# Kernel tuning notes

Hardware: AMD Instinct MI355X
Metric: run time of the kernel (lower is better)

The kernel has to match this reference:

```python
import jax, jax.numpy as jnp
import numpy as np

H, W = 512, 512          # pseudo_image_dims
C = 32                   # feat_channels == MHA embed_dim
NH, HD = 2, 16           # heads, head_dim
B, NL, NR = 2, 50000, 20000
EPS = 1e-5
SCALE = np.float32(1.0 / np.sqrt(HD))

# 3x3 neighbor shifts used by shift_bev_grids (INDEX_SHIFT in source)
INDEX_SHIFT = jnp.array([[0, 0], [-1, 0], [1, 0], [0, 1], [-1, 1], [1, 1], [0, -1], [-1, -1], [1, -1]], dtype=jnp.int32)
# 5x5 shifts used by new_gen_dy_coor (gen_index_shift(2))
SHIFT25 = jnp.array([[i, j] for i in range(-2, 3) for j in range(-2, 3)], dtype=jnp.int32)


def _unique_coords(key, n):
    perm = jax.random.permutation(key, H * W)[:n]
    return jnp.stack([perm // W, perm % W], axis=1).astype(jnp.int32)


def setup_inputs():
    key = jax.random.key(0)
    ks = jax.random.split(key, 8)
    inp = {
        "li_bev_feats": jax.random.normal(ks[0], (B, NL, C), jnp.float32),
        "li_bev_coors": jnp.stack([_unique_coords(jax.random.fold_in(ks[1], b), NL) for b in range(B)]),
        "ra_bev_feats": jax.random.normal(ks[2], (B, NR, C), jnp.float32),
        "ra_bev_coors": jnp.stack([_unique_coords(jax.random.fold_in(ks[3], b), NR) for b in range(B)]),
        "radar_bev_dy": jax.random.bernoulli(ks[4], 0.3, (B, NR)),
    }
    pk = jax.random.split(ks[5], 12)
    w = lambda k, o, i: 0.05 * jax.random.normal(k, (o, i), jnp.float32)
    z = lambda n: jnp.zeros((n,), jnp.float32)
    inp.update(
        ln_li_w=jnp.ones((C,), jnp.float32), ln_li_b=z(C),
        ln_ra_w=jnp.ones((C,), jnp.float32), ln_ra_b=z(C),
        q1_w=w(pk[0], C, C), q1_b=z(C), k1_w=w(pk[1], C, C), k1_b=z(C), v1_w=w(pk[2], C, C), v1_b=z(C),
        q2_w=w(pk[3], C, C), q2_b=z(C), k2_w=w(pk[4], C, C), k2_b=z(C), v2_w=w(pk[5], C, C), v2_b=z(C),
        pos_w=w(pk[6], C, 2), pos_b=z(C),
        a1_in_w=w(pk[7], 3 * C, C), a1_in_b=z(3 * C), a1_out_w=w(pk[8], C, C), a1_out_b=z(C),
        a2_in_w=w(pk[9], 3 * C, C), a2_in_b=z(3 * C), a2_out_w=w(pk[10], C, C), a2_out_b=z(C),
    )
    return inp


def _ln(x, w, b):
    mu = jnp.mean(x, -1, keepdims=True)
    var = jnp.mean(jnp.square(x - mu), -1, keepdims=True)
    return (x - mu) / jnp.sqrt(var + EPS) * w + b


def _grid_of(coors, n):
    # dense coord -> pillar-index lookup table, -1 for empty cells
    return jnp.full((H, W), -1, jnp.int32).at[coors[:, 0], coors[:, 1]].set(jnp.arange(n, dtype=jnp.int32))


def _gather_kv(coors, grid, k_map, v_map, pe9):
    # per pillar: look up the 3x3 shifted neighbors in the OTHER modality's grid
    sh = coors[:, None, :] + INDEX_SHIFT[None]                      # [N,9,2]
    inb = (sh[..., 0] >= 0) & (sh[..., 0] < H) & (sh[..., 1] >= 0) & (sh[..., 1] < W)
    idx = grid[jnp.clip(sh[..., 0], 0, H - 1), jnp.clip(sh[..., 1], 0, W - 1)]
    valid = (inb & (idx >= 0))[..., None]                           # [N,9,1]
    safe = jnp.clip(idx, 0, None)
    k = jnp.where(valid, k_map[safe], 0.0)                          # masked_fill(~cond, 0)
    v = jnp.where(valid, v_map[safe] + pe9[None], 0.0)              # pos-enc added before masking
    return k, v


def _mha(q, k, v, Wi, bi, Wo, bo):
    # torch MultiheadAttention (batch_first, eval -> no dropout); q [N,1,C], k/v [N,9,C]
    n = q.shape[0]
    qp = (q @ Wi[:C].T + bi[:C]).reshape(n, 1, NH, HD)
    kp = (k @ Wi[C:2 * C].T + bi[C:2 * C]).reshape(n, -1, NH, HD)
    vp = (v @ Wi[2 * C:].T + bi[2 * C:]).reshape(n, -1, NH, HD)
    s = jnp.einsum("nqhd,nkhd->nhqk", qp, kp) * SCALE
    a = jax.nn.softmax(s, axis=-1)
    o = jnp.einsum("nhqk,nkhd->nqhd", a, vp).reshape(n, C)
    return o @ Wo.T + bo


def _scatter(coors, feat):
    # PointPillarsScatter: place [N,C] features at their (x,y) cells of a [C,H,W] canvas
    return jnp.zeros((H, W, C), feat.dtype).at[coors[:, 0], coors[:, 1]].set(feat).transpose(2, 0, 1)


def _forward(li_bev_feats, li_bev_coors, ra_bev_feats, ra_bev_coors, radar_bev_dy,
             ln_li_w, ln_li_b, ln_ra_w, ln_ra_b,
             q1_w, q1_b, k1_w, k1_b, v1_w, v1_b,
             q2_w, q2_b, k2_w, k2_b, v2_w, v2_b,
             pos_w, pos_b,
             a1_in_w, a1_in_b, a1_out_w, a1_out_b,
             a2_in_w, a2_in_b, a2_out_w, a2_out_b):
    pe9 = INDEX_SHIFT.astype(jnp.float32) @ pos_w.T + pos_b        # [9,C] positional codes

    def per_sample(li_f, li_c, ra_f, ra_c, ra_dy):
        li_n = _ln(li_f, ln_li_w, ln_li_b)
        ra_n = _ln(ra_f, ln_ra_w, ln_ra_b)
        li_grid = _grid_of(li_c, NL)
        ra_grid = _grid_of(ra_c, NR)
        # new_gen_dy_coor: lidar pillars within a 5x5 (mod dims+1) window of any dynamic radar pillar
        g = jnp.array([H + 1, W + 1], jnp.int32)
        sh = (ra_c[:, None, :] + SHIFT25[None]) % g                # [NR,25,2]
        inb = (sh[..., 0] < H) & (sh[..., 1] < W)
        idx = li_grid[jnp.clip(sh[..., 0], 0, H - 1), jnp.clip(sh[..., 1], 0, W - 1)]
        valid = inb & (idx >= 0) & ra_dy[:, None]
        dy_mask = jnp.zeros(NL + 1, bool).at[jnp.where(valid, idx, NL).reshape(-1)].set(True)[:NL]
        # branch 1: dynamic lidar queries cross-attend to 3x3 radar neighbors
        q1 = li_n @ q1_w.T + q1_b
        k1 = ra_n @ k1_w.T + k1_b
        v1 = ra_n @ v1_w.T + v1_b
        k, v = _gather_kv(li_c, ra_grid, k1, v1, pe9)
        out1 = _mha(q1[:, None, :], k, v, a1_in_w, a1_in_b, a1_out_w, a1_out_b)
        out1 = out1 * dy_mask[:, None].astype(out1.dtype)          # only dy pillars scattered
        img_li = _scatter(li_c, out1)
        # branch 2: radar queries cross-attend to 3x3 lidar neighbors
        q2 = ra_n @ q2_w.T + q2_b
        k2 = li_n @ k2_w.T + k2_b
        v2 = li_n @ v2_w.T + v2_b
        k, v = _gather_kv(ra_c, li_grid, k2, v2, pe9)
        out2 = _mha(q2[:, None, :], k, v, a2_in_w, a2_in_b, a2_out_w, a2_out_b)
        img_ra = _scatter(ra_c, out2)
        return img_li, img_ra

    return jax.vmap(per_sample)(li_bev_feats, li_bev_coors, ra_bev_feats, ra_bev_coors, radar_bev_dy)


def reference(li_bev_feats, li_bev_coors, ra_bev_feats, ra_bev_coors, radar_bev_dy,
              ln_li_w, ln_li_b, ln_ra_w, ln_ra_b,
              q1_w, q1_b, k1_w, k1_b, v1_w, v1_b,
              q2_w, q2_b, k2_w, k2_b, v2_w, v2_b,
              pos_w, pos_b,
              a1_in_w, a1_in_b, a1_out_w, a1_out_b,
              a2_in_w, a2_in_b, a2_out_w, a2_out_b):
    return _forward(li_bev_feats, li_bev_coors, ra_bev_feats, ra_bev_coors, radar_bev_dy,
                    ln_li_w, ln_li_b, ln_ra_w, ln_ra_b,
                    q1_w, q1_b, k1_w, k1_b, v1_w, v1_b,
                    q2_w, q2_b, k2_w, k2_b, v2_w, v2_b,
                    pos_w, pos_b,
                    a1_in_w, a1_in_b, a1_out_w, a1_out_b,
                    a2_in_w, a2_in_b, a2_out_w, a2_out_b)
```

## Files before the change

kernel.cpp:

```cpp
#include <hip/hip_runtime.h>
#include <stdint.h>

constexpr int Hh = 512, Ww = 512;
constexpr int C  = 32;
constexpr int B  = 2;
constexpr int NL = 50000;
constexpr int NR = 20000;
constexpr float EPS = 1e-5f;
constexpr float SCALE = 0.25f;

constexpr int CB_MATS = 0;
constexpr int CB_CVEC = 6144;
constexpr int CB_PE1  = 6336;
constexpr int CB_PE2  = 6624;
constexpr int CB_INV  = 6912;
constexpr int CB_TOT  = 7040;

__device__ __constant__ int DX9[9] = {0,-1,1,0,-1,1,0,-1,1};
__device__ __constant__ int DY9[9] = {0,0,0,1,1,1,-1,-1,-1};

__global__ void build_grid_k(const int* __restrict__ coors, int n, int* __restrict__ grid) {
    int b = blockIdx.y;
    int i = blockIdx.x * blockDim.x + threadIdx.x;
    if (i >= n) return;
    int x = coors[((size_t)b * n + i) * 2 + 0];
    int y = coors[((size_t)b * n + i) * 2 + 1];
    grid[(size_t)b * Hh * Ww + x * Ww + y] = i;
}

__global__ void combine_mats_k(const float* __restrict__ a1w, const float* __restrict__ a2w,
                               const float* __restrict__ q1w, const float* __restrict__ k1w,
                               const float* __restrict__ v1w, const float* __restrict__ q2w,
                               const float* __restrict__ k2w, const float* __restrict__ v2w,
                               float* __restrict__ cb) {
    int m = blockIdx.x;
    int t = threadIdx.x;
    const float* A = (m < 3 ? a1w : a2w) + (m % 3) * C * C;
    const float* Wm;
    switch (m) { case 0: Wm=q1w; break; case 1: Wm=k1w; break; case 2: Wm=v1w; break;
                 case 3: Wm=q2w; break; case 4: Wm=k2w; break; default: Wm=v2w; }
    int r = t >> 5, d = t & 31;
    float s = 0.f;
    #pragma unroll
    for (int c = 0; c < C; ++c) s += A[r * C + c] * Wm[c * C + d];
    cb[CB_MATS + m * 1024 + r * C + d] = s;
}

__global__ void combine_vecs_k(const float* __restrict__ a1w, const float* __restrict__ a1b,
                               const float* __restrict__ a2w, const float* __restrict__ a2b,
                               const float* __restrict__ q1b, const float* __restrict__ k1b,
                               const float* __restrict__ v1b, const float* __restrict__ q2b,
                               const float* __restrict__ k2b, const float* __restrict__ v2b,
                               const float* __restrict__ posw, const float* __restrict__ posb,
                               float* __restrict__ cb) {
    int t = threadIdx.x;
    if (t < 192) {
        int m = t / 32, r = t & 31;
        const float* A  = (m < 3 ? a1w : a2w) + (m % 3) * C * C;
        const float* ab = (m < 3 ? a1b : a2b) + (m % 3) * C;
        const float* bv = (m == 0 ? q1b : m == 1 ? k1b : m == 2 ? v1b
                         : m == 3 ? q2b : m == 4 ? k2b : v2b);
        float s = ab[r];
        #pragma unroll
        for (int c = 0; c < C; ++c) s += A[r * C + c] * bv[c];
        cb[CB_CVEC + m * 32 + r] = s;
    } else if (t < 480) {
        int u = t - 192; int j = u >> 5, r = u & 31;
        const float* A = a1w + 2 * C * C;
        float sx = (float)DX9[j], sy = (float)DY9[j];
        float s = 0.f;
        #pragma unroll
        for (int c = 0; c < C; ++c) {
            float pe = posw[c * 2 + 0] * sx + posw[c * 2 + 1] * sy + posb[c];
            s += A[r * C + c] * pe;
        }
        cb[CB_PE1 + j * 32 + r] = s;
    } else if (t < 768) {
        int u = t - 480; int j = u >> 5, r = u & 31;
        const float* A = a2w + 2 * C * C;
        float sx = (float)DX9[j], sy = (float)DY9[j];
        float s = 0.f;
        #pragma unroll
        for (int c = 0; c < C; ++c) {
            float pe = posw[c * 2 + 0] * sx + posw[c * 2 + 1] * sy + posb[c];
            s += A[r * C + c] * pe;
        }
        cb[CB_PE2 + j * 32 + r] = s;
    } else if (t < 896) {
        int u = t - 768; int m = u >> 5, r = u & 31;
        cb[CB_INV + u] = (m == 0 ? a1b[32 + r] : m == 1 ? a1b[64 + r]
                        : m == 2 ? a2b[32 + r] : a2b[64 + r]);
    }
}

__global__ void ln_proj_k(const float* __restrict__ feats, int n,
                          const float* __restrict__ lnw, const float* __restrict__ lnb,
                          const float* __restrict__ cb, int mq, int mk, int mv,
                          float* __restrict__ qmap, float* __restrict__ kmap,
                          float* __restrict__ vmap) {
    __shared__ float sM[3][1024];
    __shared__ float sc[3][32];
    for (int p = threadIdx.x; p < 1024; p += blockDim.x) {
        sM[0][p] = cb[CB_MATS + mq * 1024 + p];
        sM[1][p] = cb[CB_MATS + mk * 1024 + p];
        sM[2][p] = cb[CB_MATS + mv * 1024 + p];
    }
    if (threadIdx.x < 32) {
        sc[0][threadIdx.x] = cb[CB_CVEC + mq * 32 + threadIdx.x];
        sc[1][threadIdx.x] = cb[CB_CVEC + mk * 32 + threadIdx.x];
        sc[2][threadIdx.x] = cb[CB_CVEC + mv * 32 + threadIdx.x];
    }
    __syncthreads();
    int b = blockIdx.y;
    int i = blockIdx.x * blockDim.x + threadIdx.x;
    if (i >= n) return;

    float x[C];
    const float* f = feats + ((size_t)b * n + i) * C;
    float mu = 0.f;
    #pragma unroll
    for (int c = 0; c < C; ++c) { x[c] = f[c]; mu += x[c]; }
    mu *= (1.0f / C);
    float var = 0.f;
    #pragma unroll
    for (int c = 0; c < C; ++c) { float d = x[c] - mu; var += d * d; }
    var *= (1.0f / C);
    float inv = 1.0f / sqrtf(var + EPS);
    #pragma unroll
    for (int c = 0; c < C; ++c) x[c] = (x[c] - mu) * inv * lnw[c] + lnb[c];

    float* outs[3] = { qmap, kmap, vmap };
    #pragma unroll
    for (int m = 0; m < 3; ++m) {
        float* o = outs[m] + ((size_t)b * n + i) * C;
        #pragma unroll
        for (int r = 0; r < C; ++r) {
            float s = sc[m][r];
            #pragma unroll
            for (int d = 0; d < C; ++d) s += sM[m][r * C + d] * x[d];
            o[r] = s;
        }
    }
}

__global__ void dy_mask_k(const int* __restrict__ ra_coors, const int* __restrict__ ra_dy,
                          const int* __restrict__ li_grid, uint8_t* __restrict__ mask) {
    int b = blockIdx.y;
    int r = blockIdx.x * blockDim.x + threadIdx.x;
    if (r >= NR) return;
    if (ra_dy[(size_t)b * NR + r] == 0) return;
    int x = ra_coors[((size_t)b * NR + r) * 2 + 0];
    int y = ra_coors[((size_t)b * NR + r) * 2 + 1];
    #pragma unroll
    for (int dx = -2; dx <= 2; ++dx) {
        #pragma unroll
        for (int dy = -2; dy <= 2; ++dy) {
            int sx = x + dx; sx = (sx < 0) ? sx + (Hh + 1) : (sx >= Hh + 1 ? sx - (Hh + 1) : sx);
            int sy = y + dy; sy = (sy < 0) ? sy + (Ww + 1) : (sy >= Ww + 1 ? sy - (Ww + 1) : sy);
            if (sx < Hh && sy < Ww) {
                int idx = li_grid[(size_t)b * Hh * Ww + sx * Ww + sy];
                if (idx >= 0) mask[(size_t)b * NL + idx] = 1;
            }
        }
    }
}

__global__ void attn_k(const float* __restrict__ qmap, const float* __restrict__ kmap,
                       const float* __restrict__ vmap, const int* __restrict__ q_coors,
                       const int* __restrict__ kv_grid, const float* __restrict__ cb,
                       int pe_off, int kinv_off, int vinv_off,
                       const float* __restrict__ Wo, const float* __restrict__ bo,
                       const uint8_t* __restrict__ mask, float* __restrict__ canvas,
                       int nq, int nkv) {
    __shared__ float sWo[1024];
    __shared__ float sbo[32], skinv[32], svinv[32];
    __shared__ float spe[9 * 32];
    for (int p = threadIdx.x; p < 1024; p += blockDim.x) sWo[p] = Wo[p];
    if (threadIdx.x < 32) {
        sbo[threadIdx.x]   = bo[threadIdx.x];
        skinv[threadIdx.x] = cb[kinv_off + threadIdx.x];
        svinv[threadIdx.x] = cb[vinv_off + threadIdx.x];
    }
    for (int p = threadIdx.x; p < 288; p += blockDim.x) spe[p] = cb[pe_off + p];
    __syncthreads();

    int b = blockIdx.y;
    int i = blockIdx.x * blockDim.x + threadIdx.x;
    if (i >= nq) return;
    if (mask && !mask[(size_t)b * NL + i]) return;

    int x = q_coors[((size_t)b * nq + i) * 2 + 0];
    int y = q_coors[((size_t)b * nq + i) * 2 + 1];

    int nidx[9];
    #pragma unroll
    for (int j = 0; j < 9; ++j) {
        int sx = x + DX9[j], sy = y + DY9[j];
        nidx[j] = (sx >= 0 && sx < Hh && sy >= 0 && sy < Ww)
                  ? kv_grid[(size_t)b * Hh * Ww + sx * Ww + sy] : -1;
    }

    float qp[C];
    const float* qpp = qmap + ((size_t)b * nq + i) * C;
    #pragma unroll
    for (int c = 0; c < C; ++c) qp[c] = qpp[c];

    float sc0[9], sc1[9];
    #pragma unroll
    for (int j = 0; j < 9; ++j) {
        int idx = nidx[j];
        const float* kp = (idx >= 0) ? (kmap + ((size_t)b * nkv + idx) * C) : skinv;
        float s0 = 0.f, s1 = 0.f;
        #pragma unroll
        for (int d = 0; d < 16; ++d) { s0 += qp[d] * kp[d]; s1 += qp[16 + d] * kp[16 + d]; }
        sc0[j] = s0 * SCALE; sc1[j] = s1 * SCALE;
    }
    float m0 = sc0[0], m1 = sc1[0];
    #pragma unroll
    for (int j = 1; j < 9; ++j) { m0 = fmaxf(m0, sc0[j]); m1 = fmaxf(m1, sc1[j]); }
    float sum0 = 0.f, sum1 = 0.f;
    #pragma unroll
    for (int j = 0; j < 9; ++j) {
        sc0[j] = expf(sc0[j] - m0); sum0 += sc0[j];
        sc1[j] = expf(sc1[j] - m1); sum1 += sc1[j];
    }
    float r0 = 1.0f / sum0, r1 = 1.0f / sum1;

    float o[C];
    #pragma unroll
    for (int c = 0; c < C; ++c) o[c] = 0.f;
    #pragma unroll
    for (int j = 0; j < 9; ++j) {
        float a0 = sc0[j] * r0, a1 = sc1[j] * r1;
        int idx = nidx[j];
        if (idx >= 0) {
            const float* vp = vmap + ((size_t)b * nkv + idx) * C;
            #pragma unroll
            for (int d = 0; d < 16; ++d) {
                o[d]      += a0 * (vp[d]      + spe[j * 32 + d]);
                o[16 + d] += a1 * (vp[16 + d] + spe[j * 32 + 16 + d]);
            }
        } else {
            #pragma unroll
            for (int d = 0; d < 16; ++d) {
                o[d]      += a0 * svinv[d];
                o[16 + d] += a1 * svinv[16 + d];
            }
        }
    }

    size_t base = (size_t)b * C * Hh * Ww + (size_t)x * Ww + y;
    #pragma unroll
    for (int r = 0; r < C; ++r) {
        float s = sbo[r];
        #pragma unroll
        for (int c = 0; c < C; ++c) s += sWo[r * C + c] * o[c];
        canvas[base + (size_t)r * Hh * Ww] = s;
    }
}

extern "C" void kernel_launch(void* const* d_in, const int* in_sizes, int n_in,
                              void* d_out, int out_size, void* d_ws, size_t ws_size,
                              hipStream_t stream) {
    const float*   li_f  = (const float*)d_in[0];
    const int*     li_c  = (const int*)d_in[1];
    const float*   ra_f  = (const float*)d_in[2];
    const int*     ra_c  = (const int*)d_in[3];
    const int*     ra_dy = (const int*)d_in[4];
    const float* ln_li_w = (const float*)d_in[5];
    const float* ln_li_b = (const float*)d_in[6];
    const float* ln_ra_w = (const float*)d_in[7];
    const float* ln_ra_b = (const float*)d_in[8];
    const float* q1w = (const float*)d_in[9],  *q1b = (const float*)d_in[10];
    const float* k1w = (const float*)d_in[11], *k1b = (const float*)d_in[12];
    const float* v1w = (const float*)d_in[13], *v1b = (const float*)d_in[14];
    const float* q2w = (const float*)d_in[15], *q2b = (const float*)d_in[16];
    const float* k2w = (const float*)d_in[17], *k2b = (const float*)d_in[18];
    const float* v2w = (const float*)d_in[19], *v2b = (const float*)d_in[20];
    const float* posw = (const float*)d_in[21], *posb = (const float*)d_in[22];
    const float* a1iw = (const float*)d_in[23], *a1ib = (const float*)d_in[24];
    const float* a1ow = (const float*)d_in[25], *a1ob = (const float*)d_in[26];
    const float* a2iw = (const float*)d_in[27], *a2ib = (const float*)d_in[28];
    const float* a2ow = (const float*)d_in[29], *a2ob = (const float*)d_in[30];

    char* ws = (char*)d_ws;
    size_t off = 0;
    auto carve = [&](size_t bytes) { void* p = ws + off; off += (bytes + 255) & ~(size_t)255; return p; };
    int*     li_grid = (int*)carve((size_t)B * Hh * Ww * 4);
    int*     ra_grid = (int*)carve((size_t)B * Hh * Ww * 4);
    uint8_t* mask    = (uint8_t*)carve((size_t)B * NL);
    float*   cb      = (float*)carve((size_t)CB_TOT * 4);
    float*   qp1 = (float*)carve((size_t)B * NL * C * 4);
    float*   kp1 = (float*)carve((size_t)B * NR * C * 4);
    float*   vp1 = (float*)carve((size_t)B * NR * C * 4);
    float*   qp2 = (float*)carve((size_t)B * NR * C * 4);
    float*   kp2 = (float*)carve((size_t)B * NL * C * 4);
    float*   vp2 = (float*)carve((size_t)B * NL * C * 4);
    (void)ws_size; (void)n_in; (void)in_sizes;

    float* out_li = (float*)d_out;
    float* out_ra = out_li + (size_t)B * C * Hh * Ww;

    hipMemsetAsync(d_out, 0, (size_t)out_size * sizeof(float), stream);
    hipMemsetAsync(li_grid, 0xFF, (size_t)2 * B * Hh * Ww * 4, stream);
    hipMemsetAsync(mask, 0, (size_t)B * NL, stream);

    combine_mats_k<<<dim3(6), dim3(1024), 0, stream>>>(a1iw, a2iw, q1w, k1w, v1w, q2w, k2w, v2w, cb);
    combine_vecs_k<<<dim3(1), dim3(1024), 0, stream>>>(a1iw, a1ib, a2iw, a2ib,
                                                       q1b, k1b, v1b, q2b, k2b, v2b, posw, posb, cb);
    build_grid_k<<<dim3((NL + 255) / 256, B), dim3(256), 0, stream>>>(li_c, NL, li_grid);
    build_grid_k<<<dim3((NR + 255) / 256, B), dim3(256), 0, stream>>>(ra_c, NR, ra_grid);

    ln_proj_k<<<dim3((NL + 255) / 256, B), dim3(256), 0, stream>>>(li_f, NL, ln_li_w, ln_li_b,
                                                                   cb, 0, 4, 5, qp1, kp2, vp2);
    ln_proj_k<<<dim3((NR + 255) / 256, B), dim3(256), 0, stream>>>(ra_f, NR, ln_ra_w, ln_ra_b,
                                                                   cb, 3, 1, 2, qp2, kp1, vp1);
    dy_mask_k<<<dim3((NR + 255) / 256, B), dim3(256), 0, stream>>>(ra_c, ra_dy, li_grid, mask);

    attn_k<<<dim3((NL + 255) / 256, B), dim3(256), 0, stream>>>(
        qp1, kp1, vp1, li_c, ra_grid, cb, CB_PE1, CB_INV + 0, CB_INV + 32,
        a1ow, a1ob, mask, out_li, NL, NR);
    attn_k<<<dim3((NR + 255) / 256, B), dim3(256), 0, stream>>>(
        qp2, kp2, vp2, ra_c, li_grid, cb, CB_PE2, CB_INV + 64, CB_INV + 96,
        a2ow, a2ob, nullptr, out_ra, NR, NL);
}
```

Measured before the change: 384.1 us.

## Replace output memset and strided scatter with a dense gather canvas pass

Attention kernels now write compact per-pillar features, and a new canvas kernel walks every grid cell to gather features, or write zeros, into the channel-major output. This removes the full-output memset and the scattered strided canvas writes in favour of coalesced writes. It also merges the two grid-build launches and the two constant-prep launches into one each, and uses float4 loads and stores for feature rows. The cost is extra intermediate buffers plus a pass that reads both grids and the compact features.

```diff
diff --git a/kernel.cpp b/kernel.cpp
--- a/kernel.cpp
+++ b/kernel.cpp
@@ -19,51 +19,56 @@
 __device__ __constant__ int DX9[9] = {0,-1,1,0,-1,1,0,-1,1};
 __device__ __constant__ int DY9[9] = {0,0,0,1,1,1,-1,-1,-1};
 
-__global__ void build_grid_k(const int* __restrict__ coors, int n, int* __restrict__ grid) {
+__global__ void build_grids_k(const int* __restrict__ li_c, const int* __restrict__ ra_c,
+                              int* __restrict__ li_grid, int* __restrict__ ra_grid) {
     int b = blockIdx.y;
     int i = blockIdx.x * blockDim.x + threadIdx.x;
-    if (i >= n) return;
-    int x = coors[((size_t)b * n + i) * 2 + 0];
-    int y = coors[((size_t)b * n + i) * 2 + 1];
-    grid[(size_t)b * Hh * Ww + x * Ww + y] = i;
-}
-
-__global__ void combine_mats_k(const float* __restrict__ a1w, const float* __restrict__ a2w,
-                               const float* __restrict__ q1w, const float* __restrict__ k1w,
-                               const float* __restrict__ v1w, const float* __restrict__ q2w,
-                               const float* __restrict__ k2w, const float* __restrict__ v2w,
-                               float* __restrict__ cb) {
+    if (i < NL) {
+        int x = li_c[((size_t)b * NL + i) * 2 + 0];
+        int y = li_c[((size_t)b * NL + i) * 2 + 1];
+        li_grid[(size_t)b * Hh * Ww + x * Ww + y] = i;
+    } else if (i < NL + NR) {
+        int j = i - NL;
+        int x = ra_c[((size_t)b * NR + j) * 2 + 0];
+        int y = ra_c[((size_t)b * NR + j) * 2 + 1];
+        ra_grid[(size_t)b * Hh * Ww + x * Ww + y] = j;
+    }
+}
+
+__global__ void const_k(const float* __restrict__ a1w, const float* __restrict__ a1b,
+                        const float* __restrict__ a2w, const float* __restrict__ a2b,
+                        const float* __restrict__ q1w, const float* __restrict__ q1b,
+                        const float* __restrict__ k1w, const float* __restrict__ k1b,
+                        const float* __restrict__ v1w, const float* __restrict__ v1b,
+                        const float* __restrict__ q2w, const float* __restrict__ q2b,
+                        const float* __restrict__ k2w, const float* __restrict__ k2b,
+                        const float* __restrict__ v2w, const float* __restrict__ v2b,
+                        const float* __restrict__ posw, const float* __restrict__ posb,
+                        float* __restrict__ cb) {
     int m = blockIdx.x;
     int t = threadIdx.x;
-    const float* A = (m < 3 ? a1w : a2w) + (m % 3) * C * C;
-    const float* Wm;
-    switch (m) { case 0: Wm=q1w; break; case 1: Wm=k1w; break; case 2: Wm=v1w; break;
-                 case 3: Wm=q2w; break; case 4: Wm=k2w; break; default: Wm=v2w; }
-    int r = t >> 5, d = t & 31;
-    float s = 0.f;
-    #pragma unroll
-    for (int c = 0; c < C; ++c) s += A[r * C + c] * Wm[c * C + d];
-    cb[CB_MATS + m * 1024 + r * C + d] = s;
-}
-
-__global__ void combine_vecs_k(const float* __restrict__ a1w, const float* __restrict__ a1b,
-                               const float* __restrict__ a2w, const float* __restrict__ a2b,
-                               const float* __restrict__ q1b, const float* __restrict__ k1b,
-                               const float* __restrict__ v1b, const float* __restrict__ q2b,
-                               const float* __restrict__ k2b, const float* __restrict__ v2b,
-                               const float* __restrict__ posw, const float* __restrict__ posb,
-                               float* __restrict__ cb) {
-    int t = threadIdx.x;
+    if (m < 6) {
+        const float* A = (m < 3 ? a1w : a2w) + (m % 3) * C * C;
+        const float* Wm;
+        switch (m) { case 0: Wm=q1w; break; case 1: Wm=k1w; break; case 2: Wm=v1w; break;
+                     case 3: Wm=q2w; break; case 4: Wm=k2w; break; default: Wm=v2w; }
+        int r = t >> 5, d = t & 31;
+        float s = 0.f;
+        #pragma unroll
+        for (int c = 0; c < C; ++c) s += A[r * C + c] * Wm[c * C + d];
+        cb[CB_MATS + m * 1024 + r * C + d] = s;
+        return;
+    }
     if (t < 192) {
-        int m = t / 32, r = t & 31;
-        const float* A  = (m < 3 ? a1w : a2w) + (m % 3) * C * C;
-        const float* ab = (m < 3 ? a1b : a2b) + (m % 3) * C;
-        const float* bv = (m == 0 ? q1b : m == 1 ? k1b : m == 2 ? v1b
-                         : m == 3 ? q2b : m == 4 ? k2b : v2b);
+        int mm = t / 32, r = t & 31;
+        const float* A  = (mm < 3 ? a1w : a2w) + (mm % 3) * C * C;
+        const float* ab = (mm < 3 ? a1b : a2b) + (mm % 3) * C;
+        const float* bv = (mm == 0 ? q1b : mm == 1 ? k1b : mm == 2 ? v1b
+                         : mm == 3 ? q2b : mm == 4 ? k2b : v2b);
         float s = ab[r];
         #pragma unroll
         for (int c = 0; c < C; ++c) s += A[r * C + c] * bv[c];
-        cb[CB_CVEC + m * 32 + r] = s;
+        cb[CB_CVEC + mm * 32 + r] = s;
     } else if (t < 480) {
         int u = t - 192; int j = u >> 5, r = u & 31;
         const float* A = a1w + 2 * C * C;
@@ -87,9 +92,9 @@
         }
         cb[CB_PE2 + j * 32 + r] = s;
     } else if (t < 896) {
-        int u = t - 768; int m = u >> 5, r = u & 31;
-        cb[CB_INV + u] = (m == 0 ? a1b[32 + r] : m == 1 ? a1b[64 + r]
-                        : m == 2 ? a2b[32 + r] : a2b[64 + r]);
+        int u = t - 768; int mm = u >> 5, r = u & 31;
+        cb[CB_INV + u] = (mm == 0 ? a1b[32 + r] : mm == 1 ? a1b[64 + r]
+                        : mm == 2 ? a2b[32 + r] : a2b[64 + r]);
     }
 }
 
@@ -116,10 +121,15 @@
     if (i >= n) return;
 
     float x[C];
-    const float* f = feats + ((size_t)b * n + i) * C;
+    const float4* f4 = (const float4*)(feats + ((size_t)b * n + i) * C);
+    #pragma unroll
+    for (int q = 0; q < 8; ++q) {
+        float4 t = f4[q];
+        x[4*q] = t.x; x[4*q+1] = t.y; x[4*q+2] = t.z; x[4*q+3] = t.w;
+    }
     float mu = 0.f;
     #pragma unroll
-    for (int c = 0; c < C; ++c) { x[c] = f[c]; mu += x[c]; }
+    for (int c = 0; c < C; ++c) mu += x[c];
     mu *= (1.0f / C);
     float var = 0.f;
     #pragma unroll
@@ -132,13 +142,20 @@
     float* outs[3] = { qmap, kmap, vmap };
     #pragma unroll
     for (int m = 0; m < 3; ++m) {
-        float* o = outs[m] + ((size_t)b * n + i) * C;
-        #pragma unroll
-        for (int r = 0; r < C; ++r) {
-            float s = sc[m][r];
+        float4* o4 = (float4*)(outs[m] + ((size_t)b * n + i) * C);
+        #pragma unroll
+        for (int rq = 0; rq < 8; ++rq) {
+            float4 t;
+            float* tp = &t.x;
             #pragma unroll
-            for (int d = 0; d < C; ++d) s += sM[m][r * C + d] * x[d];
-            o[r] = s;
+            for (int rr = 0; rr < 4; ++rr) {
+                int r = rq * 4 + rr;
+                float s = sc[m][r];
+                #pragma unroll
+                for (int d = 0; d < C; ++d) s += sM[m][r * C + d] * x[d];
+                tp[rr] = s;
+            }
+            o4[rq] = t;
         }
     }
 }
@@ -170,7 +187,7 @@
                        const int* __restrict__ kv_grid, const float* __restrict__ cb,
                        int pe_off, int kinv_off, int vinv_off,
                        const float* __restrict__ Wo, const float* __restrict__ bo,
-                       const uint8_t* __restrict__ mask, float* __restrict__ canvas,
+                       const uint8_t* __restrict__ mask, float* __restrict__ feat,
                        int nq, int nkv) {
     __shared__ float sWo[1024];
     __shared__ float sbo[32], skinv[32], svinv[32];
@@ -187,7 +204,13 @@
     int b = blockIdx.y;
     int i = blockIdx.x * blockDim.x + threadIdx.x;
     if (i >= nq) return;
-    if (mask && !mask[(size_t)b * NL + i]) return;
+    float4* o4 = (float4*)(feat + ((size_t)b * nq + i) * C);
+    if (mask && !mask[(size_t)b * NL + i]) {
+        float4 z = {0.f, 0.f, 0.f, 0.f};
+        #pragma unroll
+        for (int q = 0; q < 8; ++q) o4[q] = z;
+        return;
+    }
 
     int x = q_coors[((size_t)b * nq + i) * 2 + 0];
     int y = q_coors[((size_t)b * nq + i) * 2 + 1];
@@ -201,9 +224,12 @@
     }
 
     float qp[C];
-    const float* qpp = qmap + ((size_t)b * nq + i) * C;
-    #pragma unroll
-    for (int c = 0; c < C; ++c) qp[c] = qpp[c];
+    const float4* qp4 = (const float4*)(qmap + ((size_t)b * nq + i) * C);
+    #pragma unroll
+    for (int q = 0; q < 8; ++q) {
+        float4 t = qp4[q];
+        qp[4*q] = t.x; qp[4*q+1] = t.y; qp[4*q+2] = t.z; qp[4*q+3] = t.w;
+    }
 
     float sc0[9], sc1[9];
     #pragma unroll
@@ -249,14 +275,61 @@
         }
     }
 
-    size_t base = (size_t)b * C * Hh * Ww + (size_t)x * Ww + y;
-    #pragma unroll
-    for (int r = 0; r < C; ++r) {
-        float s = sbo[r];
-        #pragma unroll
-        for (int c = 0; c < C; ++c) s += sWo[r * C + c] * o[c];
-        canvas[base + (size_t)r * Hh * Ww] = s;
-    }
+    #pragma unroll
+    for (int rq = 0; rq < 8; ++rq) {
+        float4 t;
+        float* tp = &t.x;
+        #pragma unroll
+        for (int rr = 0; rr < 4; ++rr) {
+            int r = rq * 4 + rr;
+            float s = sbo[r];
+            #pragma unroll
+            for (int c = 0; c < C; ++c) s += sWo[r * C + c] * o[c];
+            tp[rr] = s;
+        }
+        o4[rq] = t;
+    }
+}
+
+__global__ void canvas_k(const int* __restrict__ li_grid, const int* __restrict__ ra_grid,
+                         const float* __restrict__ feat1, const float* __restrict__ feat2,
+                         float* __restrict__ out_li, float* __restrict__ out_ra) {
+    int b = blockIdx.y;
+    int cell = blockIdx.x * blockDim.x + threadIdx.x;
+    if (cell >= Hh * Ww) return;
+    size_t gidx = (size_t)b * Hh * Ww + cell;
+    size_t obase = (size_t)b * C * Hh * Ww + cell;
+
+    int li = li_grid[gidx];
+    float v[C];
+    if (li >= 0) {
+        const float4* f = (const float4*)(feat1 + ((size_t)b * NL + li) * C);
+        #pragma unroll
+        for (int q = 0; q < 8; ++q) {
+            float4 t = f[q];
+            v[4*q] = t.x; v[4*q+1] = t.y; v[4*q+2] = t.z; v[4*q+3] = t.w;
+        }
+    } else {
+        #pragma unroll
+        for (int c = 0; c < C; ++c) v[c] = 0.f;
+    }
+    #pragma unroll
+    for (int c = 0; c < C; ++c) out_li[obase + (size_t)c * Hh * Ww] = v[c];
+
+    int ra = ra_grid[gidx];
+    if (ra >= 0) {
+        const float4* f = (const float4*)(feat2 + ((size_t)b * NR + ra) * C);
+        #pragma unroll
+        for (int q = 0; q < 8; ++q) {
+            float4 t = f[q];
+            v[4*q] = t.x; v[4*q+1] = t.y; v[4*q+2] = t.z; v[4*q+3] = t.w;
+        }
+    } else {
+        #pragma unroll
+        for (int c = 0; c < C; ++c) v[c] = 0.f;
+    }
+    #pragma unroll
+    for (int c = 0; c < C; ++c) out_ra[obase + (size_t)c * Hh * Ww] = v[c];
 }
 
 extern "C" void kernel_launch(void* const* d_in, const int* in_sizes, int n_in,
@@ -290,26 +363,27 @@
     int*     ra_grid = (int*)carve((size_t)B * Hh * Ww * 4);
     uint8_t* mask    = (uint8_t*)carve((size_t)B * NL);
     float*   cb      = (float*)carve((size_t)CB_TOT * 4);
-    float*   qp1 = (float*)carve((size_t)B * NL * C * 4);
-    float*   kp1 = (float*)carve((size_t)B * NR * C * 4);
-    float*   vp1 = (float*)carve((size_t)B * NR * C * 4);
-    float*   qp2 = (float*)carve((size_t)B * NR * C * 4);
-    float*   kp2 = (float*)carve((size_t)B * NL * C * 4);
-    float*   vp2 = (float*)carve((size_t)B * NL * C * 4);
-    (void)ws_size; (void)n_in; (void)in_sizes;
+    float*   qp1   = (float*)carve((size_t)B * NL * C * 4);
+    float*   kp1   = (float*)carve((size_t)B * NR * C * 4);
+    float*   vp1   = (float*)carve((size_t)B * NR * C * 4);
+    float*   qp2   = (float*)carve((size_t)B * NR * C * 4);
+    float*   kp2   = (float*)carve((size_t)B * NL * C * 4);
+    float*   vp2   = (float*)carve((size_t)B * NL * C * 4);
+    float*   feat1 = (float*)carve((size_t)B * NL * C * 4);
+    float*   feat2 = (float*)carve((size_t)B * NR * C * 4);
+    (void)ws_size; (void)n_in; (void)in_sizes; (void)out_size;
 
     float* out_li = (float*)d_out;
     float* out_ra = out_li + (size_t)B * C * Hh * Ww;
 
-    hipMemsetAsync(d_out, 0, (size_t)out_size * sizeof(float), stream);
     hipMemsetAsync(li_grid, 0xFF, (size_t)2 * B * Hh * Ww * 4, stream);
     hipMemsetAsync(mask, 0, (size_t)B * NL, stream);
 
-    combine_mats_k<<<dim3(6), dim3(1024), 0, stream>>>(a1iw, a2iw, q1w, k1w, v1w, q2w, k2w, v2w, cb);
-    combine_vecs_k<<<dim3(1), dim3(1024), 0, stream>>>(a1iw, a1ib, a2iw, a2ib,
-                                                       q1b, k1b, v1b, q2b, k2b, v2b, posw, posb, cb);
-    build_grid_k<<<dim3((NL + 255) / 256, B), dim3(256), 0, stream>>>(li_c, NL, li_grid);
-    build_grid_k<<<dim3((NR + 255) / 256, B), dim3(256), 0, stream>>>(ra_c, NR, ra_grid);
+    const_k<<<dim3(7), dim3(1024), 0, stream>>>(a1iw, a1ib, a2iw, a2ib,
+                                                q1w, q1b, k1w, k1b, v1w, v1b,
+                                                q2w, q2b, k2w, k2b, v2w, v2b,
+                                                posw, posb, cb);
+    build_grids_k<<<dim3((NL + NR + 255) / 256, B), dim3(256), 0, stream>>>(li_c, ra_c, li_grid, ra_grid);
 
     ln_proj_k<<<dim3((NL + 255) / 256, B), dim3(256), 0, stream>>>(li_f, NL, ln_li_w, ln_li_b,
                                                                    cb, 0, 4, 5, qp1, kp2, vp2);
@@ -319,8 +393,11 @@
 
     attn_k<<<dim3((NL + 255) / 256, B), dim3(256), 0, stream>>>(
         qp1, kp1, vp1, li_c, ra_grid, cb, CB_PE1, CB_INV + 0, CB_INV + 32,
-        a1ow, a1ob, mask, out_li, NL, NR);
+        a1ow, a1ob, mask, feat1, NL, NR);
     attn_k<<<dim3((NR + 255) / 256, B), dim3(256), 0, stream>>>(
         qp2, kp2, vp2, ra_c, li_grid, cb, CB_PE2, CB_INV + 64, CB_INV + 96,
-        a2ow, a2ob, nullptr, out_ra, NR, NL);
-}
+        a2ow, a2ob, nullptr, feat2, NR, NL);
+
+    canvas_k<<<dim3((Hh * Ww + 255) / 256, B), dim3(256), 0, stream>>>(
+        li_grid, ra_grid, feat1, feat2, out_li, out_ra);
+}
```

New measurement: 375.2 us. -2.3%, faster.
